# Performance work log

Measured on AMD Instinct MI355X. Metric: run time of the kernel, lower is better.

Reference implementation:

```python
import jax, jax.numpy as jnp
import numpy as np

B, N, M, C = 4, 4096, 4096, 256
IMG_W, IMG_H = 1242.0, 376.0  # KITTI-like image extents for keypoint coords


def setup_inputs() -> dict:
    key = jax.random.key(0)
    ks = jax.random.split(key, 12)
    s = 1.0 / np.sqrt(C)
    scale_uv = jnp.array([IMG_W, IMG_H], dtype=jnp.float32)
    return {
        "nodes_L": jax.random.normal(ks[0], (B, N, C), jnp.float32),
        "nodes_R": jax.random.normal(ks[1], (B, M, C), jnp.float32),
        "kpts_L": jax.random.uniform(ks[2], (B, N, 2), jnp.float32) * scale_uv,
        "kpts_R": jax.random.uniform(ks[3], (B, M, 2), jnp.float32) * scale_uv,
        "Wq": jax.random.normal(ks[4], (C, C), jnp.float32) * s,
        "bq": jnp.zeros((C,), jnp.float32),
        "Wk": jax.random.normal(ks[5], (C, C), jnp.float32) * s,
        "bk": jnp.zeros((C,), jnp.float32),
        "Wv": jax.random.normal(ks[6], (C, C), jnp.float32) * s,
        "bv": jnp.zeros((C,), jnp.float32),
        "Wm": jax.random.normal(ks[7], (C, C), jnp.float32) * s,
        "bm": jnp.zeros((C,), jnp.float32),
    }


def reference(nodes_L, nodes_R, kpts_L, kpts_R, Wq, bq, Wk, bk, Wv, bv, Wm, bm):
    dim = nodes_L.shape[-1]
    # torch.nn.Linear: y = x @ W.T + b  (W is [out, in])
    Q = jnp.einsum('bnc,dc->bnd', nodes_L, Wq) + bq  # [B,N,C]
    K = jnp.einsum('bmc,dc->bmd', nodes_R, Wk) + bk  # [B,M,C]
    V = jnp.einsum('bmc,dc->bmd', nodes_R, Wv) + bv  # [B,M,C]

    # Epipolar geometric mask from keypoint coordinates
    dist_v = jnp.abs(kpts_L[:, :, 1:2] - kpts_R[:, None, :, 1])  # [B,N,M]
    dist_u = kpts_L[:, :, 0:1] - kpts_R[:, None, :, 0]           # [B,N,M]
    mask = (dist_v < 3.0) & (dist_u > 0) & (dist_u < 192)

    attn = jnp.einsum('bnd,bmd->bnm', Q, K) / (dim ** 0.5)       # [B,N,M]
    attn = jnp.where(mask, attn, jnp.float32(-1e9))
    attn_weights = jax.nn.softmax(attn, axis=-1)                 # [B,N,M]

    matched_features = jnp.einsum('bnm,bmd->bnd', attn_weights, V)
    init_disparity = jnp.sum(attn_weights * dist_u, axis=-1, keepdims=True)  # [B,N,1]
    confidence = jnp.any(mask, axis=-1, keepdims=True).astype(jnp.float32)   # [B,N,1]
    out = jnp.einsum('bnd,cd->bnc', matched_features, Wm) + bm   # [B,N,C]
    return (out, init_disparity, confidence, attn_weights)
```

## Files before the change

### kernel.cpp

```cpp
#include <hip/hip_runtime.h>
#include <stdint.h>

#define CAP 192

typedef __attribute__((ext_vector_type(4))) float f32x4;
typedef __attribute__((ext_vector_type(8))) short bf16x8;

__device__ __forceinline__ float bf2f(ushort u) {
  return __uint_as_float(((unsigned)u) << 16);
}
__device__ __forceinline__ ushort f2bf(float f) {
  unsigned u = __float_as_uint(f);
  return (ushort)((u + 0x7fffu + ((u >> 16) & 1u)) >> 16);
}
__device__ __forceinline__ float wredsum(float v) {
#pragma unroll
  for (int o = 32; o; o >>= 1) v += __shfl_xor(v, o);
  return v;
}

template <bool A_BF16, typename OutT>
__device__ __forceinline__ void gemm_body(const void* __restrict__ Av,
                                          const float* __restrict__ Wf,
                                          const float* __restrict__ bias,
                                          OutT* __restrict__ Y, int blk,
                                          ushort* As, ushort* Bs) {
  int tid = threadIdx.x;
  int lane = tid & 63, wid = tid >> 6;
  int bm = blk >> 1, bn = blk & 1;
  int r0 = bm * 128, c0 = bn * 128;
  int wr = wid >> 1, wc = wid & 1;
  f32x4 acc[4][4] = {};
  for (int k0 = 0; k0 < 256; k0 += 32) {
    __syncthreads();
#pragma unroll
    for (int p = 0; p < 2; ++p) {
      int u = p * 2048 + tid * 8;
      int row = u >> 5, col = u & 31;
      if constexpr (A_BF16) {
        *(bf16x8*)&As[u] =
            *(const bf16x8*)((const ushort*)Av + (size_t)(r0 + row) * 256 + k0 + col);
      } else {
        const float* Af = (const float*)Av;
        float4 lo = *(const float4*)(Af + (size_t)(r0 + row) * 256 + k0 + col);
        float4 hi = *(const float4*)(Af + (size_t)(r0 + row) * 256 + k0 + col + 4);
        ushort4 o0 = { f2bf(lo.x), f2bf(lo.y), f2bf(lo.z), f2bf(lo.w) };
        ushort4 o1 = { f2bf(hi.x), f2bf(hi.y), f2bf(hi.z), f2bf(hi.w) };
        *(ushort4*)&As[u] = o0;
        *(ushort4*)&As[u + 4] = o1;
      }
      {
        float4 lo = *(const float4*)(Wf + (size_t)(c0 + row) * 256 + k0 + col);
        float4 hi = *(const float4*)(Wf + (size_t)(c0 + row) * 256 + k0 + col + 4);
        ushort4 o0 = { f2bf(lo.x), f2bf(lo.y), f2bf(lo.z), f2bf(lo.w) };
        ushort4 o1 = { f2bf(hi.x), f2bf(hi.y), f2bf(hi.z), f2bf(hi.w) };
        *(ushort4*)&Bs[u] = o0;
        *(ushort4*)&Bs[u + 4] = o1;
      }
    }
    __syncthreads();
    bf16x8 af[4], bfr[4];
    int rsel = lane & 15, ksel = (lane >> 4) * 8;
#pragma unroll
    for (int m = 0; m < 4; ++m)
      af[m] = *(bf16x8*)&As[(wr * 64 + m * 16 + rsel) * 32 + ksel];
#pragma unroll
    for (int n = 0; n < 4; ++n)
      bfr[n] = *(bf16x8*)&Bs[(wc * 64 + n * 16 + rsel) * 32 + ksel];
#pragma unroll
    for (int m = 0; m < 4; ++m)
#pragma unroll
      for (int n = 0; n < 4; ++n)
        acc[m][n] = __builtin_amdgcn_mfma_f32_16x16x32_bf16(af[m], bfr[n], acc[m][n], 0, 0, 0);
  }
  int rbase = r0 + wr * 64 + ((lane >> 4) * 4);
  int cbase = c0 + wc * 64 + (lane & 15);
#pragma unroll
  for (int n = 0; n < 4; ++n) {
    float bv = bias[cbase + n * 16];
#pragma unroll
    for (int m = 0; m < 4; ++m) {
#pragma unroll
      for (int j = 0; j < 4; ++j) {
        float v = acc[m][n][j] + bv;
        size_t idx = (size_t)(rbase + m * 16 + j) * 256 + (cbase + n * 16);
        if constexpr (sizeof(OutT) == 2) Y[idx] = (OutT)f2bf(v);
        else Y[idx] = (OutT)v;
      }
    }
  }
}

__global__ __launch_bounds__(256, 2) void gemm3(
    const float* __restrict__ nodesL, const float* __restrict__ nodesR,
    const float* __restrict__ Wq, const float* __restrict__ Wk,
    const float* __restrict__ Wv, const float* __restrict__ bq,
    const float* __restrict__ bk, const float* __restrict__ bv,
    ushort* __restrict__ Qb, ushort* __restrict__ Kb, ushort* __restrict__ Vb) {
  __shared__ __align__(16) ushort As[128 * 32];
  __shared__ __align__(16) ushort Bs[128 * 32];
  int which = blockIdx.x >> 8;
  int blk = blockIdx.x & 255;
  const float* A = (which == 0) ? nodesL : nodesR;
  const float* W = (which == 0) ? Wq : (which == 1) ? Wk : Wv;
  const float* bias = (which == 0) ? bq : (which == 1) ? bk : bv;
  ushort* Y = (which == 0) ? Qb : (which == 1) ? Kb : Vb;
  gemm_body<false, ushort>(A, W, bias, Y, blk, As, Bs);
}

__global__ __launch_bounds__(256, 2) void gemm_out(const ushort* __restrict__ A,
                                                   const float* __restrict__ Wm,
                                                   const float* __restrict__ bias,
                                                   float* __restrict__ Y) {
  __shared__ __align__(16) ushort As[128 * 32];
  __shared__ __align__(16) ushort Bs[128 * 32];
  gemm_body<true, float>(A, Wm, bias, Y, blockIdx.x, As, Bs);
}

__global__ __launch_bounds__(256) void sum_nodes(const float* __restrict__ nodesR,
                                                 const float* __restrict__ kptsR,
                                                 float* __restrict__ S16,
                                                 float* __restrict__ sumU16) {
  int b = blockIdx.x >> 4, ch = blockIdx.x & 15;
  int t = threadIdx.x;
  int c4 = (t & 63) * 4;
  int r0 = b * 4096 + ch * 256 + (t >> 6);
  float4 acc = {0.f, 0.f, 0.f, 0.f};
  for (int k = 0; k < 64; ++k) {
    float4 v = *(const float4*)(nodesR + (size_t)(r0 + k * 4) * 256 + c4);
    acc.x += v.x; acc.y += v.y; acc.z += v.z; acc.w += v.w;
  }
  __shared__ float4 red[256];
  red[t] = acc;
  float u = kptsR[(size_t)(b * 4096 + ch * 256 + t) * 2];
  u = wredsum(u);
  __shared__ float ured[4];
  if ((t & 63) == 0) ured[t >> 6] = u;
  __syncthreads();
  if (t < 64) {
    float4 x = red[t], y = red[t + 64], z = red[t + 128], w = red[t + 192];
    float4 s = { x.x + y.x + z.x + w.x, x.y + y.y + z.y + w.y,
                 x.z + y.z + z.z + w.z, x.w + y.w + z.w + w.w };
    *(float4*)(S16 + (size_t)(b * 16 + ch) * 256 + t * 4) = s;
  }
  if (t == 0) sumU16[b * 16 + ch] = ured[0] + ured[1] + ured[2] + ured[3];
}

__global__ __launch_bounds__(256) void proj_mean(const float* __restrict__ S16,
                                                 const float* __restrict__ sumU16,
                                                 const float* __restrict__ Wv,
                                                 const float* __restrict__ bv,
                                                 ushort* __restrict__ meanVb,
                                                 float* __restrict__ meanU) {
  int b = blockIdx.x, c = threadIdx.x;
  __shared__ float s[256];
  float a0 = 0.f;
  for (int ch = 0; ch < 16; ++ch) a0 += S16[(size_t)(b * 16 + ch) * 256 + c];
  s[c] = a0;
  __syncthreads();
  float acc = 0.f;
  for (int k = 0; k < 256; k += 4) {
    float4 w = *(const float4*)(Wv + (size_t)c * 256 + k);
    acc += s[k] * w.x + s[k + 1] * w.y + s[k + 2] * w.z + s[k + 3] * w.w;
  }
  float mv = acc * (1.f / 4096.f) + bv[c];
  meanVb[b * 256 + c] = f2bf(mv);
  if (c == 0) {
    float su = 0.f;
    for (int ch = 0; ch < 16; ++ch) su += sumU16[b * 16 + ch];
    meanU[b] = su * (1.f / 4096.f);
  }
}

__global__ __launch_bounds__(512, 2) void attn_fused(
    const float* __restrict__ kptsL, const float* __restrict__ kptsR,
    const ushort* __restrict__ Qb, const ushort* __restrict__ Kb,
    const ushort* __restrict__ Vb, const float* __restrict__ meanU,
    const ushort* __restrict__ meanVb, float* __restrict__ disp_out,
    float* __restrict__ conf_out, ushort* __restrict__ matched,
    float* __restrict__ attn) {
  __shared__ float2 kR[4096];
  __shared__ int bufM[8][CAP];
  __shared__ float bufD[8][CAP];
  __shared__ float bufS[8][CAP];
  int tid = threadIdx.x, lane = tid & 63, wid = tid >> 6;
  int b = blockIdx.x >> 9;
  int n = ((blockIdx.x & 511) << 3) + wid;
  int row = (b << 12) + n;
  int bb = b << 12;

  float* rowp = attn + (size_t)row * 4096;
  {
    f32x4 zv = {0.f, 0.f, 0.f, 0.f};
    f32x4* dst = (f32x4*)rowp;
#pragma unroll
    for (int j = 0; j < 16; ++j)
      __builtin_nontemporal_store(zv, dst + j * 64 + lane);
  }

  const float2* kRsrc = (const float2*)kptsR + (size_t)bb;
  for (int i = tid; i < 4096; i += 512) kR[i] = kRsrc[i];
  __syncthreads();
  float2 kL = ((const float2*)kptsL)[(size_t)row];
  ushort4 qv = *(const ushort4*)(Qb + (size_t)row * 256 + lane * 4);
  float q0 = bf2f(qv.x), q1 = bf2f(qv.y), q2 = bf2f(qv.z), q3 = bf2f(qv.w);

  unsigned long long lmask = (1ull << lane) - 1ull;
  int cnt = 0;
#pragma unroll 4
  for (int m0 = 0; m0 < 4096; m0 += 64) {
    float2 kr = kR[m0 + lane];
    float dv = fabsf(kL.y - kr.y);
    float du = kL.x - kr.x;
    bool hit = (dv < 3.0f) && (du > 0.0f) && (du < 192.0f);
    unsigned long long bal = __ballot(hit);
    int pos = cnt + (int)__popcll(bal & lmask);
    if (hit && pos < CAP) { bufM[wid][pos] = m0 + lane; bufD[wid][pos] = du; }
    cnt += (int)__popcll(bal);
  }
  if (cnt > CAP) cnt = CAP;

  float conf, disp;
  if (cnt == 0) {
    conf = 0.f;
    disp = kL.x - meanU[b];
    ushort4 st = *(const ushort4*)(meanVb + b * 256 + lane * 4);
    *(ushort4*)(matched + (size_t)row * 256 + lane * 4) = st;
    asm volatile("s_waitcnt vmcnt(0)" ::: "memory");
    const float fill = 1.f / 4096.f;
    f32x4 fv = { fill, fill, fill, fill };
    f32x4* dst = (f32x4*)rowp;
#pragma unroll
    for (int j = 0; j < 16; ++j)
      __builtin_nontemporal_store(fv, dst + j * 64 + lane);
  } else {
    float mx = -1e30f;
    int i = 0;
    for (; i + 1 < cnt; i += 2) {
      int ma = bufM[wid][i], mb = bufM[wid][i + 1];
      ushort4 ka = *(const ushort4*)(Kb + ((size_t)(bb + ma)) * 256 + lane * 4);
      ushort4 kb2 = *(const ushort4*)(Kb + ((size_t)(bb + mb)) * 256 + lane * 4);
      float pa = q0 * bf2f(ka.x) + q1 * bf2f(ka.y) + q2 * bf2f(ka.z) + q3 * bf2f(ka.w);
      float pb = q0 * bf2f(kb2.x) + q1 * bf2f(kb2.y) + q2 * bf2f(kb2.z) + q3 * bf2f(kb2.w);
#pragma unroll
      for (int o = 32; o; o >>= 1) {
        pa += __shfl_xor(pa, o);
        pb += __shfl_xor(pb, o);
      }
      float sa = pa * 0.0625f, sb = pb * 0.0625f;
      if (lane == 0) { bufS[wid][i] = sa; bufS[wid][i + 1] = sb; }
      mx = fmaxf(mx, fmaxf(sa, sb));
    }
    if (i < cnt) {
      int ma = bufM[wid][i];
      ushort4 ka = *(const ushort4*)(Kb + ((size_t)(bb + ma)) * 256 + lane * 4);
      float pa = q0 * bf2f(ka.x) + q1 * bf2f(ka.y) + q2 * bf2f(ka.z) + q3 * bf2f(ka.w);
      pa = wredsum(pa);
      float sa = pa * 0.0625f;
      if (lane == 0) bufS[wid][i] = sa;
      mx = fmaxf(mx, sa);
    }
    float psum = 0.f, pdisp = 0.f;
    for (int k = lane; k < cnt; k += 64) {
      float e = expf(bufS[wid][k] - mx);
      bufS[wid][k] = e;
      psum += e;
      pdisp += e * bufD[wid][k];
    }
    psum = wredsum(psum);
    pdisp = wredsum(pdisp);
    float inv = 1.f / psum;
    disp = pdisp * inv;
    conf = 1.f;
    for (int k = lane; k < cnt; k += 64) bufS[wid][k] *= inv;
    float a0 = 0.f, a1 = 0.f, a2 = 0.f, a3 = 0.f;
    i = 0;
    for (; i + 1 < cnt; i += 2) {
      float wa = bufS[wid][i], wb = bufS[wid][i + 1];
      int ma = bufM[wid][i], mb = bufM[wid][i + 1];
      ushort4 va = *(const ushort4*)(Vb + ((size_t)(bb + ma)) * 256 + lane * 4);
      ushort4 vb2 = *(const ushort4*)(Vb + ((size_t)(bb + mb)) * 256 + lane * 4);
      a0 += wa * bf2f(va.x) + wb * bf2f(vb2.x);
      a1 += wa * bf2f(va.y) + wb * bf2f(vb2.y);
      a2 += wa * bf2f(va.z) + wb * bf2f(vb2.z);
      a3 += wa * bf2f(va.w) + wb * bf2f(vb2.w);
    }
    if (i < cnt) {
      float wa = bufS[wid][i];
      int ma = bufM[wid][i];
      ushort4 va = *(const ushort4*)(Vb + ((size_t)(bb + ma)) * 256 + lane * 4);
      a0 += wa * bf2f(va.x); a1 += wa * bf2f(va.y);
      a2 += wa * bf2f(va.z); a3 += wa * bf2f(va.w);
    }
    ushort4 st = { f2bf(a0), f2bf(a1), f2bf(a2), f2bf(a3) };
    *(ushort4*)(matched + (size_t)row * 256 + lane * 4) = st;
    asm volatile("s_waitcnt vmcnt(0)" ::: "memory");
    for (int k = lane; k < cnt; k += 64)
      rowp[bufM[wid][k]] = bufS[wid][k];
  }
  if (lane == 0) { disp_out[row] = disp; conf_out[row] = conf; }
}

extern "C" void kernel_launch(void* const* d_in, const int* in_sizes, int n_in,
                              void* d_out, int out_size, void* d_ws, size_t ws_size,
                              hipStream_t stream) {
  const float* nodes_L = (const float*)d_in[0];
  const float* nodes_R = (const float*)d_in[1];
  const float* kpts_L = (const float*)d_in[2];
  const float* kpts_R = (const float*)d_in[3];
  const float* Wq = (const float*)d_in[4];
  const float* bq = (const float*)d_in[5];
  const float* Wk = (const float*)d_in[6];
  const float* bk = (const float*)d_in[7];
  const float* Wv = (const float*)d_in[8];
  const float* bv = (const float*)d_in[9];
  const float* Wm = (const float*)d_in[10];
  const float* bm = (const float*)d_in[11];

  float* out = (float*)d_out;
  float* disp = out + 4194304;
  float* conf = disp + 16384;
  float* attn = conf + 16384;

  char* ws = (char*)d_ws;
  ushort* Qb = (ushort*)(ws + 0);
  ushort* Kb = (ushort*)(ws + 8388608);
  ushort* Vb = (ushort*)(ws + 16777216);
  ushort* matched = (ushort*)(ws + 25165824);
  float* S16 = (float*)(ws + 33554432);
  float* sumU16 = (float*)(ws + 33620224);
  float* meanU = (float*)(ws + 33620480);
  ushort* meanVb = (ushort*)(ws + 33620544);

  sum_nodes<<<64, 256, 0, stream>>>(nodes_R, kpts_R, S16, sumU16);
  gemm3<<<768, 256, 0, stream>>>(nodes_L, nodes_R, Wq, Wk, Wv, bq, bk, bv, Qb, Kb, Vb);
  proj_mean<<<4, 256, 0, stream>>>(S16, sumU16, Wv, bv, meanVb, meanU);
  attn_fused<<<2048, 512, 0, stream>>>(kpts_L, kpts_R, Qb, Kb, Vb, meanU, meanVb,
                                       disp, conf, matched, attn);
  gemm_out<<<256, 256, 0, stream>>>(matched, Wm, bm, out);
}
```

Measured before the change: 438.2 us.

## Move attention zero-fill into prep kernel, fold mean projection into GEMM, unroll gathers

Zeroing of the full attention matrix moves out of the attention kernel into a new prep kernel that also does the nodes_R column sums. The mean-V projection becomes an extra block of the QKV GEMM launch, which cuts the launch count from five to four. The K and V gather loops in the attention kernel are unrolled by four to keep more loads in flight, and the vmcnt waits that ordered the zero-fill before the sparse writes are removed. Cross-kernel stream ordering now carries that ordering, but the 256 MB zero-fill runs as its own pass instead of overlapping with attention compute.

```diff
diff --git a/kernel.cpp b/kernel.cpp
--- a/kernel.cpp
+++ b/kernel.cpp
@@ -17,6 +17,44 @@
 #pragma unroll
   for (int o = 32; o; o >>= 1) v += __shfl_xor(v, o);
   return v;
+}
+
+__global__ __launch_bounds__(256) void prep(const float* __restrict__ nodesR,
+                                            const float* __restrict__ kptsR,
+                                            float* __restrict__ S16,
+                                            float* __restrict__ sumU16,
+                                            float* __restrict__ attn) {
+  int t = threadIdx.x;
+  if (blockIdx.x < 64) {
+    int b = blockIdx.x >> 4, ch = blockIdx.x & 15;
+    int c4 = (t & 63) * 4;
+    int r0 = b * 4096 + ch * 256 + (t >> 6);
+    float4 acc = {0.f, 0.f, 0.f, 0.f};
+    for (int k = 0; k < 64; ++k) {
+      float4 v = *(const float4*)(nodesR + (size_t)(r0 + k * 4) * 256 + c4);
+      acc.x += v.x; acc.y += v.y; acc.z += v.z; acc.w += v.w;
+    }
+    __shared__ float4 red[256];
+    red[t] = acc;
+    float u = kptsR[(size_t)(b * 4096 + ch * 256 + t) * 2];
+    u = wredsum(u);
+    __shared__ float ured[4];
+    if ((t & 63) == 0) ured[t >> 6] = u;
+    __syncthreads();
+    if (t < 64) {
+      float4 x = red[t], y = red[t + 64], z = red[t + 128], w = red[t + 192];
+      float4 s = { x.x + y.x + z.x + w.x, x.y + y.y + z.y + w.y,
+                   x.z + y.z + z.z + w.z, x.w + y.w + z.w + w.w };
+      *(float4*)(S16 + (size_t)(b * 16 + ch) * 256 + t * 4) = s;
+    }
+    if (t == 0) sumU16[b * 16 + ch] = ured[0] + ured[1] + ured[2] + ured[3];
+  }
+  f32x4 z = {0.f, 0.f, 0.f, 0.f};
+  f32x4* dst = (f32x4*)attn;
+  int g = blockIdx.x * 256 + t;
+#pragma unroll
+  for (int i = 0; i < 32; ++i)
+    __builtin_nontemporal_store(z, dst + (size_t)g + (size_t)i * 524288);
 }
 
 template <bool A_BF16, typename OutT>
@@ -91,14 +129,40 @@
   }
 }
 
-__global__ __launch_bounds__(256, 2) void gemm3(
+__global__ __launch_bounds__(256, 2) void gemm3p(
     const float* __restrict__ nodesL, const float* __restrict__ nodesR,
     const float* __restrict__ Wq, const float* __restrict__ Wk,
     const float* __restrict__ Wv, const float* __restrict__ bq,
     const float* __restrict__ bk, const float* __restrict__ bv,
-    ushort* __restrict__ Qb, ushort* __restrict__ Kb, ushort* __restrict__ Vb) {
+    ushort* __restrict__ Qb, ushort* __restrict__ Kb, ushort* __restrict__ Vb,
+    const float* __restrict__ S16, const float* __restrict__ sumU16,
+    ushort* __restrict__ meanVb, float* __restrict__ meanU) {
   __shared__ __align__(16) ushort As[128 * 32];
   __shared__ __align__(16) ushort Bs[128 * 32];
+  if (blockIdx.x == 768) {
+    int c = threadIdx.x;
+    float* sf = (float*)As;
+    for (int b = 0; b < 4; ++b) {
+      float a0 = 0.f;
+      for (int ch = 0; ch < 16; ++ch) a0 += S16[(size_t)(b * 16 + ch) * 256 + c];
+      sf[c] = a0;
+      __syncthreads();
+      float acc = 0.f;
+      for (int k = 0; k < 256; k += 4) {
+        float4 w = *(const float4*)(Wv + (size_t)c * 256 + k);
+        acc += sf[k] * w.x + sf[k + 1] * w.y + sf[k + 2] * w.z + sf[k + 3] * w.w;
+      }
+      float mv = acc * (1.f / 4096.f) + bv[c];
+      meanVb[b * 256 + c] = f2bf(mv);
+      if (c == 0) {
+        float su = 0.f;
+        for (int ch = 0; ch < 16; ++ch) su += sumU16[b * 16 + ch];
+        meanU[b] = su * (1.f / 4096.f);
+      }
+      __syncthreads();
+    }
+    return;
+  }
   int which = blockIdx.x >> 8;
   int blk = blockIdx.x & 255;
   const float* A = (which == 0) ? nodesL : nodesR;
@@ -115,61 +179,6 @@
   __shared__ __align__(16) ushort As[128 * 32];
   __shared__ __align__(16) ushort Bs[128 * 32];
   gemm_body<true, float>(A, Wm, bias, Y, blockIdx.x, As, Bs);
-}
-
-__global__ __launch_bounds__(256) void sum_nodes(const float* __restrict__ nodesR,
-                                                 const float* __restrict__ kptsR,
-                                                 float* __restrict__ S16,
-                                                 float* __restrict__ sumU16) {
-  int b = blockIdx.x >> 4, ch = blockIdx.x & 15;
-  int t = threadIdx.x;
-  int c4 = (t & 63) * 4;
-  int r0 = b * 4096 + ch * 256 + (t >> 6);
-  float4 acc = {0.f, 0.f, 0.f, 0.f};
-  for (int k = 0; k < 64; ++k) {
-    float4 v = *(const float4*)(nodesR + (size_t)(r0 + k * 4) * 256 + c4);
-    acc.x += v.x; acc.y += v.y; acc.z += v.z; acc.w += v.w;
-  }
-  __shared__ float4 red[256];
-  red[t] = acc;
-  float u = kptsR[(size_t)(b * 4096 + ch * 256 + t) * 2];
-  u = wredsum(u);
-  __shared__ float ured[4];
-  if ((t & 63) == 0) ured[t >> 6] = u;
-  __syncthreads();
-  if (t < 64) {
-    float4 x = red[t], y = red[t + 64], z = red[t + 128], w = red[t + 192];
-    float4 s = { x.x + y.x + z.x + w.x, x.y + y.y + z.y + w.y,
-                 x.z + y.z + z.z + w.z, x.w + y.w + z.w + w.w };
-    *(float4*)(S16 + (size_t)(b * 16 + ch) * 256 + t * 4) = s;
-  }
-  if (t == 0) sumU16[b * 16 + ch] = ured[0] + ured[1] + ured[2] + ured[3];
-}
-
-__global__ __launch_bounds__(256) void proj_mean(const float* __restrict__ S16,
-                                                 const float* __restrict__ sumU16,
-                                                 const float* __restrict__ Wv,
-                                                 const float* __restrict__ bv,
-                                                 ushort* __restrict__ meanVb,
-                                                 float* __restrict__ meanU) {
-  int b = blockIdx.x, c = threadIdx.x;
-  __shared__ float s[256];
-  float a0 = 0.f;
-  for (int ch = 0; ch < 16; ++ch) a0 += S16[(size_t)(b * 16 + ch) * 256 + c];
-  s[c] = a0;
-  __syncthreads();
-  float acc = 0.f;
-  for (int k = 0; k < 256; k += 4) {
-    float4 w = *(const float4*)(Wv + (size_t)c * 256 + k);
-    acc += s[k] * w.x + s[k + 1] * w.y + s[k + 2] * w.z + s[k + 3] * w.w;
-  }
-  float mv = acc * (1.f / 4096.f) + bv[c];
-  meanVb[b * 256 + c] = f2bf(mv);
-  if (c == 0) {
-    float su = 0.f;
-    for (int ch = 0; ch < 16; ++ch) su += sumU16[b * 16 + ch];
-    meanU[b] = su * (1.f / 4096.f);
-  }
 }
 
 __global__ __launch_bounds__(512, 2) void attn_fused(
@@ -188,15 +197,7 @@
   int n = ((blockIdx.x & 511) << 3) + wid;
   int row = (b << 12) + n;
   int bb = b << 12;
-
   float* rowp = attn + (size_t)row * 4096;
-  {
-    f32x4 zv = {0.f, 0.f, 0.f, 0.f};
-    f32x4* dst = (f32x4*)rowp;
-#pragma unroll
-    for (int j = 0; j < 16; ++j)
-      __builtin_nontemporal_store(zv, dst + j * 64 + lane);
-  }
 
   const float2* kRsrc = (const float2*)kptsR + (size_t)bb;
   for (int i = tid; i < 4096; i += 512) kR[i] = kRsrc[i];
@@ -226,7 +227,6 @@
     disp = kL.x - meanU[b];
     ushort4 st = *(const ushort4*)(meanVb + b * 256 + lane * 4);
     *(ushort4*)(matched + (size_t)row * 256 + lane * 4) = st;
-    asm volatile("s_waitcnt vmcnt(0)" ::: "memory");
     const float fill = 1.f / 4096.f;
     f32x4 fv = { fill, fill, fill, fill };
     f32x4* dst = (f32x4*)rowp;
@@ -236,22 +236,33 @@
   } else {
     float mx = -1e30f;
     int i = 0;
-    for (; i + 1 < cnt; i += 2) {
-      int ma = bufM[wid][i], mb = bufM[wid][i + 1];
-      ushort4 ka = *(const ushort4*)(Kb + ((size_t)(bb + ma)) * 256 + lane * 4);
-      ushort4 kb2 = *(const ushort4*)(Kb + ((size_t)(bb + mb)) * 256 + lane * 4);
-      float pa = q0 * bf2f(ka.x) + q1 * bf2f(ka.y) + q2 * bf2f(ka.z) + q3 * bf2f(ka.w);
-      float pb = q0 * bf2f(kb2.x) + q1 * bf2f(kb2.y) + q2 * bf2f(kb2.z) + q3 * bf2f(kb2.w);
+    for (; i + 3 < cnt; i += 4) {
+      int m0_ = bufM[wid][i], m1_ = bufM[wid][i + 1];
+      int m2_ = bufM[wid][i + 2], m3_ = bufM[wid][i + 3];
+      ushort4 k0 = *(const ushort4*)(Kb + ((size_t)(bb + m0_)) * 256 + lane * 4);
+      ushort4 k1 = *(const ushort4*)(Kb + ((size_t)(bb + m1_)) * 256 + lane * 4);
+      ushort4 k2 = *(const ushort4*)(Kb + ((size_t)(bb + m2_)) * 256 + lane * 4);
+      ushort4 k3 = *(const ushort4*)(Kb + ((size_t)(bb + m3_)) * 256 + lane * 4);
+      float p0 = q0 * bf2f(k0.x) + q1 * bf2f(k0.y) + q2 * bf2f(k0.z) + q3 * bf2f(k0.w);
+      float p1 = q0 * bf2f(k1.x) + q1 * bf2f(k1.y) + q2 * bf2f(k1.z) + q3 * bf2f(k1.w);
+      float p2 = q0 * bf2f(k2.x) + q1 * bf2f(k2.y) + q2 * bf2f(k2.z) + q3 * bf2f(k2.w);
+      float p3 = q0 * bf2f(k3.x) + q1 * bf2f(k3.y) + q2 * bf2f(k3.z) + q3 * bf2f(k3.w);
 #pragma unroll
       for (int o = 32; o; o >>= 1) {
-        pa += __shfl_xor(pa, o);
-        pb += __shfl_xor(pb, o);
-      }
-      float sa = pa * 0.0625f, sb = pb * 0.0625f;
-      if (lane == 0) { bufS[wid][i] = sa; bufS[wid][i + 1] = sb; }
-      mx = fmaxf(mx, fmaxf(sa, sb));
-    }
-    if (i < cnt) {
+        p0 += __shfl_xor(p0, o);
+        p1 += __shfl_xor(p1, o);
+        p2 += __shfl_xor(p2, o);
+        p3 += __shfl_xor(p3, o);
+      }
+      float s0 = p0 * 0.0625f, s1 = p1 * 0.0625f;
+      float s2 = p2 * 0.0625f, s3 = p3 * 0.0625f;
+      if (lane == 0) {
+        bufS[wid][i] = s0; bufS[wid][i + 1] = s1;
+        bufS[wid][i + 2] = s2; bufS[wid][i + 3] = s3;
+      }
+      mx = fmaxf(mx, fmaxf(fmaxf(s0, s1), fmaxf(s2, s3)));
+    }
+    for (; i < cnt; ++i) {
       int ma = bufM[wid][i];
       ushort4 ka = *(const ushort4*)(Kb + ((size_t)(bb + ma)) * 256 + lane * 4);
       float pa = q0 * bf2f(ka.x) + q1 * bf2f(ka.y) + q2 * bf2f(ka.z) + q3 * bf2f(ka.w);
@@ -275,17 +286,21 @@
     for (int k = lane; k < cnt; k += 64) bufS[wid][k] *= inv;
     float a0 = 0.f, a1 = 0.f, a2 = 0.f, a3 = 0.f;
     i = 0;
-    for (; i + 1 < cnt; i += 2) {
-      float wa = bufS[wid][i], wb = bufS[wid][i + 1];
-      int ma = bufM[wid][i], mb = bufM[wid][i + 1];
-      ushort4 va = *(const ushort4*)(Vb + ((size_t)(bb + ma)) * 256 + lane * 4);
-      ushort4 vb2 = *(const ushort4*)(Vb + ((size_t)(bb + mb)) * 256 + lane * 4);
-      a0 += wa * bf2f(va.x) + wb * bf2f(vb2.x);
-      a1 += wa * bf2f(va.y) + wb * bf2f(vb2.y);
-      a2 += wa * bf2f(va.z) + wb * bf2f(vb2.z);
-      a3 += wa * bf2f(va.w) + wb * bf2f(vb2.w);
-    }
-    if (i < cnt) {
+    for (; i + 3 < cnt; i += 4) {
+      float w0 = bufS[wid][i], w1 = bufS[wid][i + 1];
+      float w2 = bufS[wid][i + 2], w3 = bufS[wid][i + 3];
+      int m0_ = bufM[wid][i], m1_ = bufM[wid][i + 1];
+      int m2_ = bufM[wid][i + 2], m3_ = bufM[wid][i + 3];
+      ushort4 v0 = *(const ushort4*)(Vb + ((size_t)(bb + m0_)) * 256 + lane * 4);
+      ushort4 v1 = *(const ushort4*)(Vb + ((size_t)(bb + m1_)) * 256 + lane * 4);
+      ushort4 v2 = *(const ushort4*)(Vb + ((size_t)(bb + m2_)) * 256 + lane * 4);
+      ushort4 v3 = *(const ushort4*)(Vb + ((size_t)(bb + m3_)) * 256 + lane * 4);
+      a0 += w0 * bf2f(v0.x) + w1 * bf2f(v1.x) + w2 * bf2f(v2.x) + w3 * bf2f(v3.x);
+      a1 += w0 * bf2f(v0.y) + w1 * bf2f(v1.y) + w2 * bf2f(v2.y) + w3 * bf2f(v3.y);
+      a2 += w0 * bf2f(v0.z) + w1 * bf2f(v1.z) + w2 * bf2f(v2.z) + w3 * bf2f(v3.z);
+      a3 += w0 * bf2f(v0.w) + w1 * bf2f(v1.w) + w2 * bf2f(v2.w) + w3 * bf2f(v3.w);
+    }
+    for (; i < cnt; ++i) {
       float wa = bufS[wid][i];
       int ma = bufM[wid][i];
       ushort4 va = *(const ushort4*)(Vb + ((size_t)(bb + ma)) * 256 + lane * 4);
@@ -294,7 +309,6 @@
     }
     ushort4 st = { f2bf(a0), f2bf(a1), f2bf(a2), f2bf(a3) };
     *(ushort4*)(matched + (size_t)row * 256 + lane * 4) = st;
-    asm volatile("s_waitcnt vmcnt(0)" ::: "memory");
     for (int k = lane; k < cnt; k += 64)
       rowp[bufM[wid][k]] = bufS[wid][k];
   }
@@ -332,9 +346,9 @@
   float* meanU = (float*)(ws + 33620480);
   ushort* meanVb = (ushort*)(ws + 33620544);
 
-  sum_nodes<<<64, 256, 0, stream>>>(nodes_R, kpts_R, S16, sumU16);
-  gemm3<<<768, 256, 0, stream>>>(nodes_L, nodes_R, Wq, Wk, Wv, bq, bk, bv, Qb, Kb, Vb);
-  proj_mean<<<4, 256, 0, stream>>>(S16, sumU16, Wv, bv, meanVb, meanU);
+  prep<<<2048, 256, 0, stream>>>(nodes_R, kpts_R, S16, sumU16, attn);
+  gemm3p<<<769, 256, 0, stream>>>(nodes_L, nodes_R, Wq, Wk, Wv, bq, bk, bv,
+                                  Qb, Kb, Vb, S16, sumU16, meanVb, meanU);
   attn_fused<<<2048, 512, 0, stream>>>(kpts_L, kpts_R, Qb, Kb, Vb, meanU, meanVb,
                                        disp, conf, matched, attn);
   gemm_out<<<256, 256, 0, stream>>>(matched, Wm, bm, out);
```

Result: slower. 474.4 us (+8.3%).
